# Optimization experiments

Hardware: AMD Instinct MI355X
Metric: run time of the kernel (lower is better)

Reference implementation:

```python
import jax, jax.numpy as jnp
import numpy as np

B, N, NTYPES, MN = 8, 1024, 2, 128
M = NTYPES * MN
BETA, M1, M2 = 8, 16, 4
NFEAT = M1 * M2
H = 128
NGHOST = 64
RMAX, RMIN = 6.0, 0.5
ENER_SHIFT = np.array([[-93.0], [-13.6]], dtype=np.float32)


def setup_inputs() -> dict:
    key = jax.random.key(0)
    ks = jax.random.split(key, 12)
    # displacement vectors with |r| in (1, Rmax-0.2)
    d = jax.random.normal(ks[0], (B, N, M, 3), jnp.float32)
    d = d / jnp.linalg.norm(d, axis=-1, keepdims=True)
    r = jax.random.uniform(ks[1], (B, N, M, 1), jnp.float32, 1.0, RMAX - 0.2)
    rvec = d * r
    list_neigh = jax.random.randint(ks[2], (B, N, NTYPES, MN), 1, N + NGHOST + 1).astype(jnp.int32)
    # sorted type map so per-type concat order matches original atom order
    Imagetype_map = jnp.concatenate([jnp.zeros(N // 2, jnp.int32), jnp.ones(N - N // 2, jnp.int32)])
    c_param = 0.1 * jax.random.normal(ks[3], (NTYPES, NTYPES, M1, BETA), jnp.float32)
    def w(k, shape):
        fan_in = shape[-2]
        return (1.0 / np.sqrt(fan_in)) * jax.random.normal(k, shape, jnp.float32)
    return {
        'list_neigh': list_neigh,
        'Imagetype_map': Imagetype_map,
        'rvec': rvec,
        'c_param': c_param,
        'W0': w(ks[4], (NTYPES, NFEAT, H)), 'b0': jnp.zeros((NTYPES, H), jnp.float32),
        'W1': w(ks[5], (NTYPES, H, H)),     'b1': jnp.zeros((NTYPES, H), jnp.float32),
        'W2': w(ks[6], (NTYPES, H, H)),     'b2': jnp.zeros((NTYPES, H), jnp.float32),
        'Wout': w(ks[7], (NTYPES, H, 1)),   'bout': jnp.asarray(ENER_SHIFT),
    }


def _cheb(u):
    # Chebyshev polynomials T_0..T_{BETA-1}, stacked on last axis
    Ts = [jnp.ones_like(u), u]
    for _ in range(2, BETA):
        Ts.append(2.0 * u * Ts[-1] - Ts[-2])
    return jnp.stack(Ts[:BETA], axis=-1)


def _features(rvec, Imagetype_map, c_param):
    r = jnp.linalg.norm(rvec, axis=-1)                      # (B,N,M)
    valid = r > 1e-6
    r_safe = jnp.where(valid, r, 1.0)
    span = RMAX - RMIN
    u = jnp.clip(2.0 * (r_safe - RMIN) / span - 1.0, -1.0, 1.0)
    fc = jnp.where(valid & (r_safe < RMAX),
                   0.5 * (jnp.cos(jnp.pi * (jnp.clip(r_safe, RMIN, RMAX) - RMIN) / span) + 1.0),
                   0.0)
    T = _cheb(u)                                            # (B,N,M,BETA)
    # per-pair Chebyshev coefficients c[type_i, type_j, m1, k]; neighbor type is the block index
    c_i = c_param[Imagetype_map]                            # (N, NTYPES, M1, BETA)
    c_pair = jnp.repeat(c_i, MN, axis=1)                    # (N, M, M1, BETA)
    g = jnp.einsum('bnmk,nmpk->bnmp', T, c_pair) * fc[..., None]   # (B,N,M,M1)
    unit = rvec / r_safe[..., None]
    q = jnp.concatenate([jnp.ones_like(r_safe)[..., None], unit], axis=-1)  # (B,N,M,4)
    q = q * valid[..., None]
    S = jnp.einsum('bnmp,bnma->bnpa', g, q) / M             # (B,N,M1,4)
    feat = jnp.einsum('bnpa,bnqa->bnpq', S, S[:, :, :M2])   # (B,N,M1,M2)
    return feat.reshape(feat.shape[0], feat.shape[1], NFEAT)


def _normalize(feat, Imagetype_map):
    # per-type StandardScaler over all feat values of atoms of that type (detached)
    means, stds = [], []
    for t in range(NTYPES):
        w = (Imagetype_map == t).astype(feat.dtype)         # (N,)
        cnt = w.sum() * feat.shape[0] * NFEAT
        mu = (feat * w[None, :, None]).sum() / cnt
        var = (((feat - mu) ** 2) * w[None, :, None]).sum() / (cnt - 1.0)
        means.append(mu)
        stds.append(jnp.sqrt(var))
    means = jax.lax.stop_gradient(jnp.stack(means))
    stds = jax.lax.stop_gradient(jnp.stack(stds))
    mt = means[Imagetype_map][None, :, None]
    st = stds[Imagetype_map][None, :, None]
    return (feat - mt) / st


def _fit(feat_n, Imagetype_map, W0, b0, W1, b1, W2, b2, Wout, bout):
    Ei = jnp.zeros(feat_n.shape[:2] + (1,), feat_n.dtype)
    for t in range(NTYPES):
        h = jnp.tanh(feat_n @ W0[t] + b0[t])
        h = jnp.tanh(h @ W1[t] + b1[t]) + h                 # resnet skip (equal dims)
        h = jnp.tanh(h @ W2[t] + b2[t]) + h
        e = h @ Wout[t] + bout[t]                           # (B,N,1)
        Ei = Ei + e * (Imagetype_map == t)[None, :, None]
    return Ei


def reference(list_neigh, Imagetype_map, rvec, c_param, W0, b0, W1, b1, W2, b2, Wout, bout):
    def ei_fn(rv):
        feat = _features(rv, Imagetype_map, c_param)
        feat_n = _normalize(feat, Imagetype_map)
        return _fit(feat_n, Imagetype_map, W0, b0, W1, b1, W2, b2, Wout, bout)

    Ei = ei_fn(rvec)                                        # (B,N,1)
    Etot = Ei.sum(axis=1)                                   # (B,1)

    # forces / virial: dE/d rij, scatter-add to center & neighbor atoms (incl. ghosts)
    dEdr = jax.grad(lambda rv: ei_fn(rv).sum())(rvec)       # (B,N,M,3)
    Force = jnp.zeros((B, N + NGHOST, 3), rvec.dtype)
    Force = Force.at[:, :N].add(dEdr.sum(axis=2))           # center atoms: F_i = +sum_j dE/drij
    nl = list_neigh.reshape(B, N, M)
    valid = nl > 0
    j = jnp.where(valid, nl - 1, 0)
    flat_idx = (jnp.arange(B)[:, None, None] * (N + NGHOST) + j).reshape(-1)
    contrib = jnp.where(valid[..., None], -dEdr, 0.0).reshape(-1, 3)
    Force = Force.reshape(-1, 3).at[flat_idx].add(contrib).reshape(B, N + NGHOST, 3)
    Virial = -jnp.einsum('bnma,bnmc->bac', rvec, dEdr).reshape(B, 9)
    return (Etot, Ei.squeeze(-1), Force, Virial)
```

## Files before the change

kernel.cpp:

```cpp
#include <hip/hip_runtime.h>
#include <math.h>

#define BB 8
#define NN 1024
#define MM 256
#define BETA 8
#define M1 16
#define NFEAT 64
#define HH 128
#define NTOT 1088
#define F3 (NTOT*3)
#define RMINf 0.5f
#define SPANf 5.5f
#define PIf 3.14159265358979323846f

#define OUT_EI 8
#define OUT_FORCE 8200
#define OUT_VIR 34312

#define NG2 128
#define AT2 (NN/NG2)

#define MT 16
#define AS0 68
#define AS1 132

#define FEAT_BLKS 2048

#define WS_S     0
#define WS_DF    (WS_S + 8192*64)
#define WS_STATP (WS_DF + 8192*64)
#define WS_WTB   (WS_STATP + 8192*2)
#define WS_WB    (WS_WTB + 40960)
#define WT0_OFF  0
#define WT1_OFF  16384
#define WT2_OFF  49152

typedef __attribute__((ext_vector_type(8))) short bf8;
typedef __attribute__((ext_vector_type(4))) float f4;

__device__ __forceinline__ float ftanh(float x) {
  const float e = __expf(2.0f*x);
  return 1.0f - 2.0f/(e + 1.0f);
}
__device__ __forceinline__ short f2bs(float f) {
  unsigned u = __float_as_uint(f);
  return (short)((u + 0x7FFFu + ((u >> 16) & 1u)) >> 16);
}
__device__ __forceinline__ bf8 a_frag(const float* p) {
  bf8 a;
  #pragma unroll
  for (int i = 0; i < 8; ++i) a[i] = f2bs(p[i]);
  return a;
}
__device__ __forceinline__ f4 splat4(float v) {
  f4 r; r[0] = v; r[1] = v; r[2] = v; r[3] = v; return r;
}
__device__ __forceinline__ float dpp_wave_sum(float x) {
  x += __int_as_float(__builtin_amdgcn_update_dpp(0, __float_as_int(x), 0x111, 0xf, 0xf, true));
  x += __int_as_float(__builtin_amdgcn_update_dpp(0, __float_as_int(x), 0x112, 0xf, 0xf, true));
  x += __int_as_float(__builtin_amdgcn_update_dpp(0, __float_as_int(x), 0x114, 0xf, 0xf, true));
  x += __int_as_float(__builtin_amdgcn_update_dpp(0, __float_as_int(x), 0x118, 0xf, 0xf, true));
  x += __int_as_float(__builtin_amdgcn_update_dpp(0, __float_as_int(x), 0x142, 0xf, 0xf, true));
  x += __int_as_float(__builtin_amdgcn_update_dpp(0, __float_as_int(x), 0x143, 0xf, 0xf, true));
  return x;
}

__global__ __launch_bounds__(256) void k_feat(
    const float* __restrict__ rvec, const int* __restrict__ tmap,
    const float* __restrict__ c_param, float* __restrict__ S_ws,
    float* __restrict__ statp,
    const float* __restrict__ W0, const float* __restrict__ W1,
    const float* __restrict__ W2,
    unsigned short* __restrict__ wtb, unsigned short* __restrict__ wb)
{
  const int tid = threadIdx.x;
  if (blockIdx.x >= FEAT_BLKS) {
    const int idx = (blockIdx.x - FEAT_BLKS)*256 + tid;
    if (idx < 81920) {
      unsigned short v;
      if (idx < 16384) {
        const int t = idx >> 13, rem = idx & 8191;
        const int j = rem >> 6, f = rem & 63;
        v = (unsigned short)f2bs(W0[t*8192 + f*128 + j]);
      } else if (idx < 49152) {
        const int i = idx - 16384;
        const int t = i >> 14, rem = i & 16383;
        const int j = rem >> 7, f = rem & 127;
        v = (unsigned short)f2bs(W1[t*16384 + f*128 + j]);
      } else {
        const int i = idx - 49152;
        const int t = i >> 14, rem = i & 16383;
        const int j = rem >> 7, f = rem & 127;
        v = (unsigned short)f2bs(W2[t*16384 + f*128 + j]);
      }
      wtb[idx] = v;
    } else {
      const int k = idx - 81920;
      float src;
      if (k < 16384) src = W0[k];
      else if (k < 49152) src = W1[k - 16384];
      else src = W2[k - 49152];
      wb[k] = (unsigned short)f2bs(src);
    }
    return;
  }
  __shared__ float cA[512];
  __shared__ float Ubuf[4*64];
  __shared__ float Slds[4*64];
  cA[tid] = c_param[tid];
  cA[256 + tid] = c_param[256 + tid];
  __syncthreads();

  const int wave = tid >> 6, lane = tid & 63;
  const int bn = blockIdx.x*4 + wave;
  const int n = bn & (NN-1);
  const int ti = tmap[n];
  const float* rb = rvec + (size_t)bn*MM*3;

  #pragma unroll
  for (int half = 0; half < 2; ++half) {
    float acc[32];
    #pragma unroll
    for (int c = 0; c < 32; ++c) acc[c] = 0.f;
    #pragma unroll
    for (int s = 0; s < 2; ++s) {
      const int m = half*128 + s*64 + lane;
      const float x = rb[3*m], y = rb[3*m+1], z = rb[3*m+2];
      const float r = sqrtf(x*x + y*y + z*z);
      const float ir = 1.0f/r;
      const float ux = x*ir, uy = y*ir, uz = z*ir;
      float u = 2.0f*(r - RMINf)/SPANf - 1.0f;
      u = fminf(fmaxf(u, -1.0f), 1.0f);
      const float fc = 0.5f*(__cosf(PIf*(r - RMINf)/SPANf) + 1.0f);
      float tm2 = 1.0f, tm1 = u;
      acc[0] += fc;  acc[1] += fc*ux;  acc[2] += fc*uy;  acc[3] += fc*uz;
      {
        const float ft = fc*u;
        acc[4] += ft; acc[5] += ft*ux; acc[6] += ft*uy; acc[7] += ft*uz;
      }
      #pragma unroll
      for (int k = 2; k < BETA; ++k) {
        const float tk = 2.0f*u*tm1 - tm2;
        const float ft = fc*tk;
        acc[k*4+0] += ft;
        acc[k*4+1] += ft*ux;
        acc[k*4+2] += ft*uy;
        acc[k*4+3] += ft*uz;
        tm2 = tm1; tm1 = tk;
      }
    }
    #pragma unroll
    for (int c = 0; c < 32; ++c) acc[c] = dpp_wave_sum(acc[c]);
    if (lane == 63) {
      float* Uw = &Ubuf[wave*64 + half*32];
      #pragma unroll
      for (int c = 0; c < 32; ++c) Uw[c] = acc[c];
    }
  }
  {
    const int p = lane >> 2, a = lane & 3;
    const float* Uw = &Ubuf[wave*64];
    const float* cw = &cA[ti*256];
    float s = 0.f;
    #pragma unroll
    for (int tj = 0; tj < 2; ++tj)
      #pragma unroll
      for (int k = 0; k < 8; ++k)
        s += cw[tj*128 + p*8 + k] * Uw[tj*32 + k*4 + a];
    s *= (1.0f/(float)MM);
    Slds[wave*64 + lane] = s;
    S_ws[(size_t)bn*64 + lane] = s;
  }
  {
    const int p = lane >> 2, q = lane & 3;
    const float* Sw = &Slds[wave*64];
    float f = 0.f;
    #pragma unroll
    for (int a = 0; a < 4; ++a) f += Sw[p*4+a]*Sw[q*4+a];
    float fs = f, fss = f*f;
    for (int o = 32; o > 0; o >>= 1) { fs += __shfl_down(fs, o); fss += __shfl_down(fss, o); }
    if (lane == 0) { statp[bn*2+0] = fs; statp[bn*2+1] = fss; }
  }
}

__global__ __launch_bounds__(256) void k_mlp(
    const float* __restrict__ S_ws, const int* __restrict__ tmap,
    const float* __restrict__ statp,
    const unsigned short* __restrict__ wtb, const unsigned short* __restrict__ wb,
    const float* __restrict__ b0, const float* __restrict__ b1,
    const float* __restrict__ b2, const float* __restrict__ Wout,
    const float* __restrict__ bout,
    float* __restrict__ dfeat_ws, float* __restrict__ out)
{
  __shared__ float sl[MT*64];
  __shared__ float xb[MT*AS0];
  __shared__ float t0b[MT*AS1];
  __shared__ float h1b[MT*AS1];
  __shared__ float dzb[MT*AS1];
  __shared__ float es[MT];
  __shared__ float srd[8];
  __shared__ float muSd[2];
  const int tb = blockIdx.x;
  const int bn0 = tb*MT;
  const int tid = threadIdx.x;
  const int wave = tid >> 6, lane = tid & 63;
  const int quad = lane >> 4, nI = lane & 15;
  const int t = tmap[bn0 & (NN-1)];
  {
    const float4* src = (const float4*)(S_ws + (size_t)bn0*64);
    ((float4*)sl)[tid] = src[tid];
  }
  {
    float fs = 0.f, fss = 0.f;
    #pragma unroll 4
    for (int i = 0; i < 16; ++i) {
      const int e = i*256 + tid;
      const int b = e >> 9;
      const int n = t*512 + (e & 511);
      const float2 v = *(const float2*)&statp[((size_t)(b*NN + n))*2];
      fs += v.x; fss += v.y;
    }
    for (int o = 32; o > 0; o >>= 1) { fs += __shfl_down(fs, o); fss += __shfl_down(fss, o); }
    if ((tid & 63) == 0) { srd[(tid>>6)*2] = fs; srd[(tid>>6)*2+1] = fss; }
  }
  __syncthreads();
  if (tid == 0) {
    const float S1 = srd[0]+srd[2]+srd[4]+srd[6];
    const float S2 = srd[1]+srd[3]+srd[5]+srd[7];
    const float cnt = 512.0f * (float)BB * (float)NFEAT;
    const float mu = S1/cnt;
    const float var = (S2 - cnt*mu*mu)/(cnt - 1.0f);
    muSd[0] = mu; muSd[1] = sqrtf(fmaxf(var, 1e-20f));
  }
  __syncthreads();
  const float mu = muSd[0];
  const float inv_sd = 1.0f/muSd[1];
  #pragma unroll
  for (int i = 0; i < 4; ++i) {
    const int e = i*256 + tid;
    const int at = e >> 6, f = e & 63;
    const int p = f >> 2, q = f & 3;
    const float* Sr = &sl[at*64];
    float s = 0.f;
    #pragma unroll
    for (int a = 0; a < 4; ++a) s += Sr[p*4+a]*Sr[q*4+a];
    xb[at*AS0 + f] = (s - mu)*inv_sd;
  }
  __syncthreads();

  const int c0 = (wave*2+0)*16 + nI;
  const int c1 = (wave*2+1)*16 + nI;
  f4 acc0, acc1;

  acc0 = splat4(b0[t*HH + c0]);
  acc1 = splat4(b0[t*HH + c1]);
  {
    const unsigned short* B = wtb + WT0_OFF + t*8192;
    #pragma unroll
    for (int s = 0; s < 2; ++s) {
      const bf8 a  = a_frag(&xb[nI*AS0 + s*32 + quad*8]);
      const bf8 bA = *(const bf8*)&B[(size_t)c0*64 + s*32 + quad*8];
      const bf8 bB = *(const bf8*)&B[(size_t)c1*64 + s*32 + quad*8];
      acc0 = __builtin_amdgcn_mfma_f32_16x16x32_bf16(a, bA, acc0, 0, 0, 0);
      acc1 = __builtin_amdgcn_mfma_f32_16x16x32_bf16(a, bB, acc1, 0, 0, 0);
    }
  }
  #pragma unroll
  for (int r = 0; r < 4; ++r) {
    const int row = quad*4 + r;
    t0b[row*AS1 + c0] = ftanh(acc0[r]);
    t0b[row*AS1 + c1] = ftanh(acc1[r]);
  }
  __syncthreads();
  acc0 = splat4(b1[t*HH + c0]);
  acc1 = splat4(b1[t*HH + c1]);
  {
    const unsigned short* B = wtb + WT1_OFF + t*16384;
    #pragma unroll
    for (int s = 0; s < 4; ++s) {
      const bf8 a  = a_frag(&t0b[nI*AS1 + s*32 + quad*8]);
      const bf8 bA = *(const bf8*)&B[(size_t)c0*128 + s*32 + quad*8];
      const bf8 bB = *(const bf8*)&B[(size_t)c1*128 + s*32 + quad*8];
      acc0 = __builtin_amdgcn_mfma_f32_16x16x32_bf16(a, bA, acc0, 0, 0, 0);
      acc1 = __builtin_amdgcn_mfma_f32_16x16x32_bf16(a, bB, acc1, 0, 0, 0);
    }
  }
  #pragma unroll
  for (int r = 0; r < 4; ++r) {
    const int row = quad*4 + r;
    h1b[row*AS1 + c0] = ftanh(acc0[r]) + t0b[row*AS1 + c0];
    h1b[row*AS1 + c1] = ftanh(acc1[r]) + t0b[row*AS1 + c1];
  }
  __syncthreads();
  acc0 = splat4(b2[t*HH + c0]);
  acc1 = splat4(b2[t*HH + c1]);
  {
    const unsigned short* B = wtb + WT2_OFF + t*16384;
    #pragma unroll
    for (int s = 0; s < 4; ++s) {
      const bf8 a  = a_frag(&h1b[nI*AS1 + s*32 + quad*8]);
      const bf8 bA = *(const bf8*)&B[(size_t)c0*128 + s*32 + quad*8];
      const bf8 bB = *(const bf8*)&B[(size_t)c1*128 + s*32 + quad*8];
      acc0 = __builtin_amdgcn_mfma_f32_16x16x32_bf16(a, bA, acc0, 0, 0, 0);
      acc1 = __builtin_amdgcn_mfma_f32_16x16x32_bf16(a, bB, acc1, 0, 0, 0);
    }
  }
  #pragma unroll
  for (int r = 0; r < 4; ++r) {
    const int row = quad*4 + r;
    dzb[row*AS1 + c0] = acc0[r];
    dzb[row*AS1 + c1] = acc1[r];
  }
  __syncthreads();
  {
    const int at = tid >> 4, cb = (tid & 15)*8;
    const float* wop = Wout + t*HH;
    float ep = 0.f;
    #pragma unroll
    for (int j = 0; j < 8; ++j) {
      const int c = cb + j;
      const float z2 = dzb[at*AS1 + c];
      const float t2 = ftanh(z2);
      const float wo = wop[c];
      ep += (t2 + h1b[at*AS1 + c])*wo;
      dzb[at*AS1 + c] = wo*(1.0f - t2*t2);
    }
    ep += __shfl_down(ep, 8, 16);
    ep += __shfl_down(ep, 4, 16);
    ep += __shfl_down(ep, 2, 16);
    ep += __shfl_down(ep, 1, 16);
    if ((tid & 15) == 0) es[at] = ep;
  }
  __syncthreads();
  if (tid < MT) out[OUT_EI + bn0 + tid] = es[tid] + bout[t];
  if (tid == 0) {
    float s = 0.f;
    #pragma unroll
    for (int i = 0; i < MT; ++i) s += es[i];
    atomicAdd(&out[bn0 >> 10], s + (float)MT*bout[t]);
  }

  {
    const float* wop = Wout + t*HH;
    acc0 = splat4(wop[c0]);
    acc1 = splat4(wop[c1]);
    const unsigned short* B = wb + WT2_OFF + t*16384;
    #pragma unroll
    for (int s = 0; s < 4; ++s) {
      const bf8 a  = a_frag(&dzb[nI*AS1 + s*32 + quad*8]);
      const bf8 bA = *(const bf8*)&B[(size_t)c0*128 + s*32 + quad*8];
      const bf8 bB = *(const bf8*)&B[(size_t)c1*128 + s*32 + quad*8];
      acc0 = __builtin_amdgcn_mfma_f32_16x16x32_bf16(a, bA, acc0, 0, 0, 0);
      acc1 = __builtin_amdgcn_mfma_f32_16x16x32_bf16(a, bB, acc1, 0, 0, 0);
    }
  }
  __syncthreads();
  float dh10[4], dh11[4];
  #pragma unroll
  for (int r = 0; r < 4; ++r) {
    const int row = quad*4 + r;
    dh10[r] = acc0[r]; dh11[r] = acc1[r];
    const float t1a = h1b[row*AS1 + c0] - t0b[row*AS1 + c0];
    const float t1b = h1b[row*AS1 + c1] - t0b[row*AS1 + c1];
    dzb[row*AS1 + c0] = acc0[r]*(1.0f - t1a*t1a);
    dzb[row*AS1 + c1] = acc1[r]*(1.0f - t1b*t1b);
  }
  __syncthreads();
  acc0[0]=dh10[0]; acc0[1]=dh10[1]; acc0[2]=dh10[2]; acc0[3]=dh10[3];
  acc1[0]=dh11[0]; acc1[1]=dh11[1]; acc1[2]=dh11[2]; acc1[3]=dh11[3];
  {
    const unsigned short* B = wb + WT1_OFF + t*16384;
    #pragma unroll
    for (int s = 0; s < 4; ++s) {
      const bf8 a  = a_frag(&dzb[nI*AS1 + s*32 + quad*8]);
      const bf8 bA = *(const bf8*)&B[(size_t)c0*128 + s*32 + quad*8];
      const bf8 bB = *(const bf8*)&B[(size_t)c1*128 + s*32 + quad*8];
      acc0 = __builtin_amdgcn_mfma_f32_16x16x32_bf16(a, bA, acc0, 0, 0, 0);
      acc1 = __builtin_amdgcn_mfma_f32_16x16x32_bf16(a, bB, acc1, 0, 0, 0);
    }
  }
  __syncthreads();
  #pragma unroll
  for (int r = 0; r < 4; ++r) {
    const int row = quad*4 + r;
    const float ta = t0b[row*AS1 + c0], tb = t0b[row*AS1 + c1];
    dzb[row*AS1 + c0] = acc0[r]*(1.0f - ta*ta);
    dzb[row*AS1 + c1] = acc1[r]*(1.0f - tb*tb);
  }
  __syncthreads();
  {
    const int cx = wave*16 + nI;
    acc0 = splat4(0.f);
    const unsigned short* B = wb + WT0_OFF + t*8192;
    #pragma unroll
    for (int s = 0; s < 4; ++s) {
      const bf8 a  = a_frag(&dzb[nI*AS1 + s*32 + quad*8]);
      const bf8 bA = *(const bf8*)&B[(size_t)cx*128 + s*32 + quad*8];
      acc0 = __builtin_amdgcn_mfma_f32_16x16x32_bf16(a, bA, acc0, 0, 0, 0);
    }
    #pragma unroll
    for (int r = 0; r < 4; ++r)
      dfeat_ws[(size_t)(bn0 + quad*4 + r)*64 + cx] = acc0[r]*inv_sd;
  }
}

__global__ __launch_bounds__(256, 4) void k_bwdsc(
    const float* __restrict__ rvec, const int* __restrict__ nlist,
    const int* __restrict__ tmap, const float* __restrict__ c_param,
    const float* __restrict__ S_ws, const float* __restrict__ dfeat_ws,
    float* __restrict__ out)
{
  __shared__ float c_lds[256];
  __shared__ float Sb[AT2*64];
  __shared__ float Db[AT2*64];
  __shared__ float dSb[AT2*64];
  __shared__ float Eb[AT2*64];
  __shared__ float fpart[F3];
  __shared__ float wredc[AT2*4*3];
  __shared__ float vred[4*9];
  const int blk = blockIdx.x;
  const int b = blk >> 7;
  const int g = blk & (NG2-1);
  const int n0 = g*AT2;
  const int tid = threadIdx.x;
  const int ti = tmap[n0];
  c_lds[tid] = c_param[ti*256 + tid];
  if (tid < 128) {
    const float4* s4 = (const float4*)(S_ws + ((size_t)b*NN + n0)*64);
    const float4* d4 = (const float4*)(dfeat_ws + ((size_t)b*NN + n0)*64);
    ((float4*)Sb)[tid] = s4[tid];
    ((float4*)Db)[tid] = d4[tid];
  }
  {
    const float4 z4 = {0.f, 0.f, 0.f, 0.f};
    for (int i = tid; i < F3/4; i += 256) ((float4*)fpart)[i] = z4;
  }
  __syncthreads();
  #pragma unroll
  for (int it = 0; it < 2; ++it) {
    const int idx = it*256 + tid;
    const int at = idx >> 6, f = idx & 63;
    const int i = f >> 2, a = f & 3;
    const float* Sr = &Sb[at*64];
    const float* Dr = &Db[at*64];
    float v = 0.f;
    #pragma unroll
    for (int q = 0; q < 4; ++q) v += Dr[i*4+q]*Sr[q*4+a];
    if (i < 4)
      for (int p = 0; p < 16; ++p) v += Dr[p*4+i]*Sr[p*4+a];
    dSb[idx] = v;
  }
  __syncthreads();
  #pragma unroll
  for (int it = 0; it < 2; ++it) {
    const int idx = it*256 + tid;
    const int at = idx >> 6, rem = idx & 63;
    const int tj = rem >> 5, a = (rem >> 3) & 3, k = rem & 7;
    float e = 0.f;
    #pragma unroll
    for (int p = 0; p < 16; ++p) e += dSb[at*64 + p*4 + a]*c_lds[tj*128 + p*8 + k];
    Eb[idx] = e;
  }
  __syncthreads();

  float vir[9];
  #pragma unroll
  for (int i = 0; i < 9; ++i) vir[i] = 0.f;
  const int wave = tid >> 6, lane = tid & 63;
  const int tjm = tid >> 7;
  const float dudr = 2.0f/SPANf;
  const float invM = 1.0f/(float)MM;

  const size_t rowbase = ((size_t)b*NN + n0)*MM;
  float px0, py0, pz0, px1, py1, pz1; int pnl0, pnl1;
  {
    const float* rp0 = rvec + (rowbase + tid)*3;
    const float* rp1 = rvec + (rowbase + MM + tid)*3;
    px0 = rp0[0]; py0 = rp0[1]; pz0 = rp0[2]; pnl0 = nlist[rowbase + tid];
    px1 = rp1[0]; py1 = rp1[1]; pz1 = rp1[2]; pnl1 = nlist[rowbase + MM + tid];
  }
  for (int a0 = 0; a0 < AT2; a0 += 2) {
    const float x0 = px0, y0 = py0, z0 = pz0; const int nl0 = pnl0;
    const float x1 = px1, y1 = py1, z1 = pz1; const int nl1 = pnl1;
    if (a0 + 2 < AT2) {
      const float* rp0 = rvec + (rowbase + (size_t)(a0+2)*MM + tid)*3;
      const float* rp1 = rvec + (rowbase + (size_t)(a0+3)*MM + tid)*3;
      px0 = rp0[0]; py0 = rp0[1]; pz0 = rp0[2];
      pnl0 = nlist[rowbase + (size_t)(a0+2)*MM + tid];
      px1 = rp1[0]; py1 = rp1[1]; pz1 = rp1[2];
      pnl1 = nlist[rowbase + (size_t)(a0+3)*MM + tid];
    }
    float Er0[32], Er1[32];
    {
      const float4* p0 = (const float4*)&Eb[a0*64 + tjm*32];
      const float4* p1 = (const float4*)&Eb[(a0+1)*64 + tjm*32];
      #pragma unroll
      for (int q = 0; q < 8; ++q) {
        const float4 v0 = p0[q], v1 = p1[q];
        Er0[q*4+0]=v0.x; Er0[q*4+1]=v0.y; Er0[q*4+2]=v0.z; Er0[q*4+3]=v0.w;
        Er1[q*4+0]=v1.x; Er1[q*4+1]=v1.y; Er1[q*4+2]=v1.z; Er1[q*4+3]=v1.w;
      }
    }
    const float r_0 = sqrtf(x0*x0 + y0*y0 + z0*z0);
    const float r_1 = sqrtf(x1*x1 + y1*y1 + z1*z1);
    const float ir0 = 1.0f/r_0, ir1 = 1.0f/r_1;
    const float ux0 = x0*ir0, uy0 = y0*ir0, uz0 = z0*ir0;
    const float ux1 = x1*ir1, uy1 = y1*ir1, uz1 = z1*ir1;
    float u0 = 2.0f*(r_0 - RMINf)/SPANf - 1.0f;
    float u1 = 2.0f*(r_1 - RMINf)/SPANf - 1.0f;
    u0 = fminf(fmaxf(u0, -1.0f), 1.0f);
    u1 = fminf(fmaxf(u1, -1.0f), 1.0f);
    float s0a, c0a, s1a, c1a;
    __sincosf(PIf*(r_0 - RMINf)/SPANf, &s0a, &c0a);
    __sincosf(PIf*(r_1 - RMINf)/SPANf, &s1a, &c1a);
    const float fc0 = 0.5f*(c0a + 1.0f), dfc0 = -0.5f*(PIf/SPANf)*s0a;
    const float fc1 = 0.5f*(c1a + 1.0f), dfc1 = -0.5f*(PIf/SPANf)*s1a;
    float ta0[4], tda0[4], ta1[4], tda1[4];
    #pragma unroll
    for (int aa = 0; aa < 4; ++aa) {
      ta0[aa]  = Er0[aa*8] + Er0[aa*8+1]*u0;
      tda0[aa] = Er0[aa*8+1];
      ta1[aa]  = Er1[aa*8] + Er1[aa*8+1]*u1;
      tda1[aa] = Er1[aa*8+1];
    }
    float t0m2 = 1.f, t0m1 = u0, d0m2 = 0.f, d0m1 = 1.f;
    float t1m2 = 1.f, t1m1 = u1, d1m2 = 0.f, d1m1 = 1.f;
    #pragma unroll
    for (int k = 2; k < BETA; ++k) {
      const float tk0 = 2.f*u0*t0m1 - t0m2;
      const float dk0 = 2.f*t0m1 + 2.f*u0*d0m1 - d0m2;
      const float tk1 = 2.f*u1*t1m1 - t1m2;
      const float dk1 = 2.f*t1m1 + 2.f*u1*d1m1 - d1m2;
      #pragma unroll
      for (int aa = 0; aa < 4; ++aa) {
        ta0[aa]  += Er0[aa*8+k]*tk0;
        tda0[aa] += Er0[aa*8+k]*dk0;
        ta1[aa]  += Er1[aa*8+k]*tk1;
        tda1[aa] += Er1[aa*8+k]*dk1;
      }
      t0m2 = t0m1; t0m1 = tk0; d0m2 = d0m1; d0m1 = dk0;
      t1m2 = t1m1; t1m1 = tk1; d1m2 = d1m1; d1m1 = dk1;
    }
    float A0 = dfc0*(ta0[0] + ux0*ta0[1] + uy0*ta0[2] + uz0*ta0[3])
             + fc0*dudr*(tda0[0] + ux0*tda0[1] + uy0*tda0[2] + uz0*tda0[3]);
    float A1 = dfc1*(ta1[0] + ux1*ta1[1] + uy1*ta1[2] + uz1*ta1[3])
             + fc1*dudr*(tda1[0] + ux1*tda1[1] + uy1*tda1[2] + uz1*tda1[3]);
    float q10 = fc0*ta0[1], q20 = fc0*ta0[2], q30 = fc0*ta0[3];
    float q11 = fc1*ta1[1], q21 = fc1*ta1[2], q31 = fc1*ta1[3];
    A0 *= invM; q10 *= invM; q20 *= invM; q30 *= invM;
    A1 *= invM; q11 *= invM; q21 *= invM; q31 *= invM;
    const float qu0 = q10*ux0 + q20*uy0 + q30*uz0;
    const float qu1 = q11*ux1 + q21*uy1 + q31*uz1;
    const float d00 = A0*ux0 + (q10 - qu0*ux0)*ir0;
    const float d01 = A0*uy0 + (q20 - qu0*uy0)*ir0;
    const float d02 = A0*uz0 + (q30 - qu0*uz0)*ir0;
    const float d10 = A1*ux1 + (q11 - qu1*ux1)*ir1;
    const float d11 = A1*uy1 + (q21 - qu1*uy1)*ir1;
    const float d12 = A1*uz1 + (q31 - qu1*uz1)*ir1;
    if (nl0 > 0) {
      const int j = nl0 - 1;
      atomicAdd(&fpart[j*3+0], -d00);
      atomicAdd(&fpart[j*3+1], -d01);
      atomicAdd(&fpart[j*3+2], -d02);
    }
    if (nl1 > 0) {
      const int j = nl1 - 1;
      atomicAdd(&fpart[j*3+0], -d10);
      atomicAdd(&fpart[j*3+1], -d11);
      atomicAdd(&fpart[j*3+2], -d12);
    }
    vir[0] -= x0*d00 + x1*d10; vir[1] -= x0*d01 + x1*d11; vir[2] -= x0*d02 + x1*d12;
    vir[3] -= y0*d00 + y1*d10; vir[4] -= y0*d01 + y1*d11; vir[5] -= y0*d02 + y1*d12;
    vir[6] -= z0*d00 + z1*d10; vir[7] -= z0*d01 + z1*d11; vir[8] -= z0*d02 + z1*d12;
    const float r00 = dpp_wave_sum(d00), r01 = dpp_wave_sum(d01), r02 = dpp_wave_sum(d02);
    const float r10 = dpp_wave_sum(d10), r11 = dpp_wave_sum(d11), r12 = dpp_wave_sum(d12);
    if (lane == 63) {
      wredc[(a0*4 + wave)*3 + 0] = r00;
      wredc[(a0*4 + wave)*3 + 1] = r01;
      wredc[(a0*4 + wave)*3 + 2] = r02;
      wredc[((a0+1)*4 + wave)*3 + 0] = r10;
      wredc[((a0+1)*4 + wave)*3 + 1] = r11;
      wredc[((a0+1)*4 + wave)*3 + 2] = r12;
    }
  }
  #pragma unroll
  for (int i = 0; i < 9; ++i) {
    const float v = dpp_wave_sum(vir[i]);
    if (lane == 63) vred[wave*9 + i] = v;
  }
  __syncthreads();
  if (tid < AT2*3) {
    const int at = tid/3, c = tid - at*3;
    const float v = wredc[(at*4+0)*3+c] + wredc[(at*4+1)*3+c]
                  + wredc[(at*4+2)*3+c] + wredc[(at*4+3)*3+c];
    atomicAdd(&fpart[(n0+at)*3 + c], v);
  }
  if (tid >= 64 && tid < 73) {
    const int i = tid - 64;
    atomicAdd(&out[OUT_VIR + b*9 + i],
              vred[i] + vred[9+i] + vred[18+i] + vred[27+i]);
  }
  __syncthreads();
  {
    float* dst = out + OUT_FORCE + (size_t)b*F3;
    for (int i = tid; i < F3; i += 256)
      atomicAdd(&dst[i], fpart[i]);
  }
}

extern "C" void kernel_launch(void* const* d_in, const int* in_sizes, int n_in,
                              void* d_out, int out_size, void* d_ws, size_t ws_size,
                              hipStream_t stream)
{
  const int*   nlist = (const int*)d_in[0];
  const int*   tmap  = (const int*)d_in[1];
  const float* rvec  = (const float*)d_in[2];
  const float* cpar  = (const float*)d_in[3];
  const float* W0 = (const float*)d_in[4];
  const float* b0 = (const float*)d_in[5];
  const float* W1 = (const float*)d_in[6];
  const float* b1 = (const float*)d_in[7];
  const float* W2 = (const float*)d_in[8];
  const float* b2 = (const float*)d_in[9];
  const float* Wout = (const float*)d_in[10];
  const float* bout = (const float*)d_in[11];
  float* out = (float*)d_out;
  float* ws = (float*)d_ws;
  float* S_ws   = ws + WS_S;
  float* df_ws  = ws + WS_DF;
  float* statp  = ws + WS_STATP;
  unsigned short* wtb = (unsigned short*)(ws + WS_WTB);
  unsigned short* wb  = (unsigned short*)(ws + WS_WB);

  hipMemsetAsync(d_out, 0, (size_t)out_size, stream);

  k_feat <<<FEAT_BLKS + 640, 256, 0, stream>>>(rvec, tmap, cpar, S_ws, statp,
                                               W0, W1, W2, wtb, wb);
  k_mlp  <<<(BB*NN)/MT, 256, 0, stream>>>(S_ws, tmap, statp, wtb, wb,
                                          b0, b1, b2, Wout, bout, df_ws, out);
  k_bwdsc<<<BB*NG2, 256, 0, stream>>>(rvec, nlist, tmap, cpar, S_ws, df_ws,
                                      out);
}
```

Baseline: 172.9 us.

## Fuse MLP and backward-scatter kernels into one per-tile kernel

Merges the MLP forward/backward kernel with the force/virial backward-scatter kernel, so each 16-atom block feeds its feature gradient straight through shared memory. This removes the dfeat workspace round trip through global memory and one kernel launch. It also halves the number of per-block global force atomic flushes. In exchange, the scatter phase now runs with half as many blocks (16 atoms each) and a lower occupancy bound. That may reduce latency hiding for the large rvec/neighbor-list stream.

```diff
diff --git a/kernel.cpp b/kernel.cpp
--- a/kernel.cpp
+++ b/kernel.cpp
@@ -18,23 +18,33 @@
 #define OUT_FORCE 8200
 #define OUT_VIR 34312
 
-#define NG2 128
-#define AT2 (NN/NG2)
-
 #define MT 16
+#define FUSE_BLKS ((BB*NN)/MT)
 #define AS0 68
 #define AS1 132
 
 #define FEAT_BLKS 2048
 
 #define WS_S     0
-#define WS_DF    (WS_S + 8192*64)
-#define WS_STATP (WS_DF + 8192*64)
+#define WS_STATP (WS_S + 8192*64)
 #define WS_WTB   (WS_STATP + 8192*2)
 #define WS_WB    (WS_WTB + 40960)
 #define WT0_OFF  0
 #define WT1_OFF  16384
 #define WT2_OFF  49152
+
+#define SL_O  0
+#define XB_O  1024
+#define T0_O  2112
+#define H1_O  4224
+#define DZ_O  6336
+#define CL_O  8448
+#define ES_O  8704
+#define SRD_O 8720
+#define MU_O  8728
+#define WR_O  8730
+#define VR_O  8922
+#define SM_TOT 8958
 
 typedef __attribute__((ext_vector_type(8))) short bf8;
 typedef __attribute__((ext_vector_type(4))) float f4;
@@ -184,29 +194,39 @@
   }
 }
 
-__global__ __launch_bounds__(256) void k_mlp(
+__global__ __launch_bounds__(256, 2) void k_fused(
     const float* __restrict__ S_ws, const int* __restrict__ tmap,
     const float* __restrict__ statp,
     const unsigned short* __restrict__ wtb, const unsigned short* __restrict__ wb,
     const float* __restrict__ b0, const float* __restrict__ b1,
     const float* __restrict__ b2, const float* __restrict__ Wout,
     const float* __restrict__ bout,
-    float* __restrict__ dfeat_ws, float* __restrict__ out)
+    const float* __restrict__ rvec, const int* __restrict__ nlist,
+    const float* __restrict__ c_param,
+    float* __restrict__ out)
 {
-  __shared__ float sl[MT*64];
-  __shared__ float xb[MT*AS0];
-  __shared__ float t0b[MT*AS1];
-  __shared__ float h1b[MT*AS1];
-  __shared__ float dzb[MT*AS1];
-  __shared__ float es[MT];
-  __shared__ float srd[8];
-  __shared__ float muSd[2];
+  __shared__ float sm[SM_TOT];
+  float* sl   = sm + SL_O;
+  float* xb   = sm + XB_O;
+  float* t0b  = sm + T0_O;
+  float* h1b  = sm + H1_O;
+  float* dzb  = sm + DZ_O;
+  float* c_lds= sm + CL_O;
+  float* es   = sm + ES_O;
+  float* srd  = sm + SRD_O;
+  float* muSd = sm + MU_O;
+  float* wredc= sm + WR_O;
+  float* vred = sm + VR_O;
+
   const int tb = blockIdx.x;
   const int bn0 = tb*MT;
+  const int b = bn0 >> 10;
+  const int n0l = bn0 & (NN-1);
   const int tid = threadIdx.x;
   const int wave = tid >> 6, lane = tid & 63;
   const int quad = lane >> 4, nI = lane & 15;
-  const int t = tmap[bn0 & (NN-1)];
+  const int t = tmap[n0l];
+  c_lds[tid] = c_param[t*256 + tid];
   {
     const float4* src = (const float4*)(S_ws + (size_t)bn0*64);
     ((float4*)sl)[tid] = src[tid];
@@ -216,9 +236,9 @@
     #pragma unroll 4
     for (int i = 0; i < 16; ++i) {
       const int e = i*256 + tid;
-      const int b = e >> 9;
+      const int bb = e >> 9;
       const int n = t*512 + (e & 511);
-      const float2 v = *(const float2*)&statp[((size_t)(b*NN + n))*2];
+      const float2 v = *(const float2*)&statp[((size_t)(bb*NN + n))*2];
       fs += v.x; fss += v.y;
     }
     for (int o = 32; o > 0; o >>= 1) { fs += __shfl_down(fs, o); fss += __shfl_down(fss, o); }
@@ -338,7 +358,7 @@
     float s = 0.f;
     #pragma unroll
     for (int i = 0; i < MT; ++i) s += es[i];
-    atomicAdd(&out[bn0 >> 10], s + (float)MT*bout[t]);
+    atomicAdd(&out[b], s + (float)MT*bout[t]);
   }
 
   {
@@ -384,9 +404,9 @@
   #pragma unroll
   for (int r = 0; r < 4; ++r) {
     const int row = quad*4 + r;
-    const float ta = t0b[row*AS1 + c0], tb = t0b[row*AS1 + c1];
+    const float ta = t0b[row*AS1 + c0], tb2 = t0b[row*AS1 + c1];
     dzb[row*AS1 + c0] = acc0[r]*(1.0f - ta*ta);
-    dzb[row*AS1 + c1] = acc1[r]*(1.0f - tb*tb);
+    dzb[row*AS1 + c1] = acc1[r]*(1.0f - tb2*tb2);
   }
   __syncthreads();
   {
@@ -399,80 +419,64 @@
       const bf8 bA = *(const bf8*)&B[(size_t)cx*128 + s*32 + quad*8];
       acc0 = __builtin_amdgcn_mfma_f32_16x16x32_bf16(a, bA, acc0, 0, 0, 0);
     }
+    __syncthreads();
+    float* Db = dzb;
     #pragma unroll
     for (int r = 0; r < 4; ++r)
-      dfeat_ws[(size_t)(bn0 + quad*4 + r)*64 + cx] = acc0[r]*inv_sd;
-  }
-}
-
-__global__ __launch_bounds__(256, 4) void k_bwdsc(
-    const float* __restrict__ rvec, const int* __restrict__ nlist,
-    const int* __restrict__ tmap, const float* __restrict__ c_param,
-    const float* __restrict__ S_ws, const float* __restrict__ dfeat_ws,
-    float* __restrict__ out)
-{
-  __shared__ float c_lds[256];
-  __shared__ float Sb[AT2*64];
-  __shared__ float Db[AT2*64];
-  __shared__ float dSb[AT2*64];
-  __shared__ float Eb[AT2*64];
-  __shared__ float fpart[F3];
-  __shared__ float wredc[AT2*4*3];
-  __shared__ float vred[4*9];
-  const int blk = blockIdx.x;
-  const int b = blk >> 7;
-  const int g = blk & (NG2-1);
-  const int n0 = g*AT2;
-  const int tid = threadIdx.x;
-  const int ti = tmap[n0];
-  c_lds[tid] = c_param[ti*256 + tid];
-  if (tid < 128) {
-    const float4* s4 = (const float4*)(S_ws + ((size_t)b*NN + n0)*64);
-    const float4* d4 = (const float4*)(dfeat_ws + ((size_t)b*NN + n0)*64);
-    ((float4*)Sb)[tid] = s4[tid];
-    ((float4*)Db)[tid] = d4[tid];
-  }
+      Db[(quad*4 + r)*64 + cx] = acc0[r]*inv_sd;
+  }
+  __syncthreads();
+
+  {
+    float* dSb = t0b;
+    const float* Db = dzb;
+    #pragma unroll
+    for (int it = 0; it < 4; ++it) {
+      const int idx = it*256 + tid;
+      const int at = idx >> 6, f = idx & 63;
+      const int i = f >> 2, a = f & 3;
+      const float* Sr = &sl[at*64];
+      const float* Dr = &Db[at*64];
+      float v = 0.f;
+      #pragma unroll
+      for (int q = 0; q < 4; ++q) v += Dr[i*4+q]*Sr[q*4+a];
+      if (i < 4)
+        for (int p = 0; p < 16; ++p) v += Dr[p*4+i]*Sr[p*4+a];
+      dSb[idx] = v;
+    }
+  }
+  __syncthreads();
+  {
+    float* Eb = h1b;
+    const float* dSb = t0b;
+    #pragma unroll
+    for (int it = 0; it < 4; ++it) {
+      const int idx = it*256 + tid;
+      const int at = idx >> 6, rem = idx & 63;
+      const int tj = rem >> 5, a = (rem >> 3) & 3, k = rem & 7;
+      float e = 0.f;
+      #pragma unroll
+      for (int p = 0; p < 16; ++p) e += dSb[at*64 + p*4 + a]*c_lds[tj*128 + p*8 + k];
+      Eb[idx] = e;
+    }
+  }
+  __syncthreads();
   {
     const float4 z4 = {0.f, 0.f, 0.f, 0.f};
-    for (int i = tid; i < F3/4; i += 256) ((float4*)fpart)[i] = z4;
-  }
-  __syncthreads();
-  #pragma unroll
-  for (int it = 0; it < 2; ++it) {
-    const int idx = it*256 + tid;
-    const int at = idx >> 6, f = idx & 63;
-    const int i = f >> 2, a = f & 3;
-    const float* Sr = &Sb[at*64];
-    const float* Dr = &Db[at*64];
-    float v = 0.f;
-    #pragma unroll
-    for (int q = 0; q < 4; ++q) v += Dr[i*4+q]*Sr[q*4+a];
-    if (i < 4)
-      for (int p = 0; p < 16; ++p) v += Dr[p*4+i]*Sr[p*4+a];
-    dSb[idx] = v;
-  }
-  __syncthreads();
-  #pragma unroll
-  for (int it = 0; it < 2; ++it) {
-    const int idx = it*256 + tid;
-    const int at = idx >> 6, rem = idx & 63;
-    const int tj = rem >> 5, a = (rem >> 3) & 3, k = rem & 7;
-    float e = 0.f;
-    #pragma unroll
-    for (int p = 0; p < 16; ++p) e += dSb[at*64 + p*4 + a]*c_lds[tj*128 + p*8 + k];
-    Eb[idx] = e;
-  }
-  __syncthreads();
-
+    for (int i = tid; i < F3/4; i += 256) ((float4*)sm)[i] = z4;
+  }
+  __syncthreads();
+
+  float* fpart = sm;
+  const float* Eb = h1b;
   float vir[9];
   #pragma unroll
   for (int i = 0; i < 9; ++i) vir[i] = 0.f;
-  const int wave = tid >> 6, lane = tid & 63;
   const int tjm = tid >> 7;
   const float dudr = 2.0f/SPANf;
   const float invM = 1.0f/(float)MM;
 
-  const size_t rowbase = ((size_t)b*NN + n0)*MM;
+  const size_t rowbase = (size_t)bn0*MM;
   float px0, py0, pz0, px1, py1, pz1; int pnl0, pnl1;
   {
     const float* rp0 = rvec + (rowbase + tid)*3;
@@ -480,10 +484,10 @@
     px0 = rp0[0]; py0 = rp0[1]; pz0 = rp0[2]; pnl0 = nlist[rowbase + tid];
     px1 = rp1[0]; py1 = rp1[1]; pz1 = rp1[2]; pnl1 = nlist[rowbase + MM + tid];
   }
-  for (int a0 = 0; a0 < AT2; a0 += 2) {
+  for (int a0 = 0; a0 < MT; a0 += 2) {
     const float x0 = px0, y0 = py0, z0 = pz0; const int nl0 = pnl0;
     const float x1 = px1, y1 = py1, z1 = pz1; const int nl1 = pnl1;
-    if (a0 + 2 < AT2) {
+    if (a0 + 2 < MT) {
       const float* rp0 = rvec + (rowbase + (size_t)(a0+2)*MM + tid)*3;
       const float* rp1 = rvec + (rowbase + (size_t)(a0+3)*MM + tid)*3;
       px0 = rp0[0]; py0 = rp0[1]; pz0 = rp0[2];
@@ -590,11 +594,11 @@
     if (lane == 63) vred[wave*9 + i] = v;
   }
   __syncthreads();
-  if (tid < AT2*3) {
+  if (tid < MT*3) {
     const int at = tid/3, c = tid - at*3;
     const float v = wredc[(at*4+0)*3+c] + wredc[(at*4+1)*3+c]
                   + wredc[(at*4+2)*3+c] + wredc[(at*4+3)*3+c];
-    atomicAdd(&fpart[(n0+at)*3 + c], v);
+    atomicAdd(&fpart[(n0l+at)*3 + c], v);
   }
   if (tid >= 64 && tid < 73) {
     const int i = tid - 64;
@@ -628,7 +632,6 @@
   float* out = (float*)d_out;
   float* ws = (float*)d_ws;
   float* S_ws   = ws + WS_S;
-  float* df_ws  = ws + WS_DF;
   float* statp  = ws + WS_STATP;
   unsigned short* wtb = (unsigned short*)(ws + WS_WTB);
   unsigned short* wb  = (unsigned short*)(ws + WS_WB);
@@ -637,8 +640,7 @@
 
   k_feat <<<FEAT_BLKS + 640, 256, 0, stream>>>(rvec, tmap, cpar, S_ws, statp,
                                                W0, W1, W2, wtb, wb);
-  k_mlp  <<<(BB*NN)/MT, 256, 0, stream>>>(S_ws, tmap, statp, wtb, wb,
-                                          b0, b1, b2, Wout, bout, df_ws, out);
-  k_bwdsc<<<BB*NG2, 256, 0, stream>>>(rvec, nlist, tmap, cpar, S_ws, df_ws,
-                                      out);
-}
+  k_fused<<<FUSE_BLKS, 256, 0, stream>>>(S_ws, tmap, statp, wtb, wb,
+                                         b0, b1, b2, Wout, bout,
+                                         rvec, nlist, cpar, out);
+}
```

Measured after the change: 168.0 us, median of 2. 1.03x faster.
